# Optimization experiments

Hardware: AMD Instinct MI355X
Metric: run time of the kernel (lower is better)

## Reference

```python
import jax, jax.numpy as jnp
import numpy as np

B = 131072
NUM_MODS = 6
NUM_PREDS = 30
CLS_TH = 2.0
CLS_IGNORE = 0.2
MGN = 0.2
CLS_COEF = 1.0
REG_COEF = 1.0


def setup_inputs() -> dict:
    key = jax.random.key(0)
    k1, k2, k3 = jax.random.split(key, 3)
    reg = jax.random.normal(k1, (B, NUM_MODS, NUM_PREDS, 2), jnp.float32)
    cls = jax.random.normal(k2, (B, NUM_MODS), jnp.float32)
    gt_preds = jax.random.normal(k3, (B, NUM_PREDS, 2), jnp.float32)
    has_preds = jnp.ones((B, NUM_PREDS), dtype=bool)
    return {"reg": reg, "cls": cls, "gt_preds": gt_preds, "has_preds": has_preds}


def _loss(reg, cls, gt, has):
    # ---------------- PredLoss (LaneGCN cls + reg loss) ----------------
    hasf = has.astype(jnp.float32)
    last = hasf + 0.1 * jnp.arange(NUM_PREDS, dtype=jnp.float32) / float(NUM_PREDS)
    last_idcs = jnp.argmax(last, axis=1)                      # [B]
    max_last = jnp.max(last, axis=1)
    valid = max_last > 1.0                                    # [B] rows kept by `mask`

    # distance of each mode's last-valid point to gt last-valid point
    reg_last = jnp.take_along_axis(reg, last_idcs[:, None, None, None], axis=2)[:, :, 0, :]  # [B,6,2]
    gt_last = jnp.take_along_axis(gt, last_idcs[:, None, None], axis=1)[:, 0, :]             # [B,2]
    dist = jnp.sqrt(((reg_last - gt_last[:, None, :]) ** 2).sum(-1))                          # [B,6]

    min_idcs = jnp.argmin(dist, axis=1)                       # [B]
    min_dist = jnp.min(dist, axis=1)

    cls_min = jnp.take_along_axis(cls, min_idcs[:, None], axis=1)  # [B,1]
    mgn = cls_min - cls                                            # [B,6]
    m01 = (min_dist < CLS_TH)[:, None] & ((dist - min_dist[:, None]) > CLS_IGNORE) & valid[:, None]
    cls_mask = m01 & (mgn < MGN)
    num_cls = cls_mask.sum()
    cls_loss = CLS_COEF * (MGN * num_cls.astype(jnp.float32) - jnp.where(cls_mask, mgn, 0.0).sum())

    # SmoothL1 (beta=1, reduction='sum') over best mode, masked by has & valid
    reg_best = jnp.take_along_axis(reg, min_idcs[:, None, None, None], axis=1)[:, 0]  # [B,30,2]
    diff = reg_best - gt
    ad = jnp.abs(diff)
    sl1 = jnp.where(ad < 1.0, 0.5 * diff * diff, ad - 0.5)
    w = (has & valid[:, None]).astype(jnp.float32)[..., None]  # [B,30,1]
    reg_loss = REG_COEF * (sl1 * w).sum()
    num_reg = (has & valid[:, None]).sum()

    loss = cls_loss / (num_cls.astype(jnp.float32) + 1e-10) + reg_loss / (num_reg.astype(jnp.float32) + 1e-10)

    # ---------------- heading (vectorized over scenes) ----------------
    gx, gy = gt[..., 0], gt[..., 1]                           # [B,30]
    fwd = jnp.arctan2(gy[:, 2:] - gy[:, 1:-1], gx[:, 2:] - gx[:, 1:-1])   # [B,28]
    bwd = jnp.arctan2(gy[:, 1:-1] - gy[:, :-2], gx[:, 1:-1] - gx[:, :-2]) # [B,28]
    head_tmp = jnp.rad2deg(fwd) + jnp.rad2deg(bwd)                         # [B,28]
    mid = jnp.where((fwd == 0.0) | (bwd == 0.0), head_tmp, head_tmp / 2.0)
    head0 = jnp.rad2deg(jnp.arctan2(gy[:, 1] - gy[:, 0], gx[:, 1] - gx[:, 0]))
    headL = jnp.rad2deg(jnp.arctan2(gy[:, -1] - gy[:, -2], gx[:, -1] - gx[:, -2]))
    head = jnp.concatenate([head0[:, None], mid, headL[:, None]], axis=1)  # [B,30]
    moving = jnp.sqrt(((gt[:, 0, :] - gt[:, -1, :]) ** 2).sum(-1)) > 2.0
    head = jnp.where(moving[:, None], head, 0.0)

    # ---------------- rotated dist_error (per-timestep 2x2 rotation) ----------------
    de0 = jnp.abs(gt[:, None, :, :] - reg)                    # [B,6,30,2] L1Loss(reduction='none')
    theta = jnp.deg2rad(-head)                                # [B,30]
    c = jnp.cos(theta)[:, None, :]                            # [B,1,30]
    s = jnp.sin(theta)[:, None, :]
    dx, dy = de0[..., 0], de0[..., 1]                         # [B,6,30]
    rx = c * dx - s * dy
    ry = s * dx + c * dy
    de = jnp.abs(jnp.stack([rx, ry], axis=-1))                # [B,6,30,2]

    top1 = jnp.argmax(cls, axis=1)                            # [B]
    de_top = jnp.take_along_axis(de, top1[:, None, None, None], axis=1)[:, 0]  # [B,30,2]

    ade6_x = de[..., 0].sum(); ade6_y = de[..., 1].sum()
    fde6_x = de[:, :, -1, 0].sum(); fde6_y = de[:, :, -1, 1].sum()
    ade1_x = de_top[..., 0].sum(); ade1_y = de_top[..., 1].sum()
    fde1_x = de_top[:, -1, 0].sum(); fde1_y = de_top[:, -1, 1].sum()

    Bn = de.shape[0]
    counts = jnp.array([
        NUM_MODS * Bn * NUM_PREDS,  # ade6_num
        NUM_MODS * Bn,              # fde6_num
        Bn * NUM_PREDS,             # ade1_num
        Bn,                         # fde1_num
    ], dtype=jnp.float32)

    return jnp.stack([
        loss, cls_loss, num_cls.astype(jnp.float32), reg_loss, num_reg.astype(jnp.float32),
        ade6_x, ade6_y, fde6_x, fde6_y, counts[0], counts[1],
        ade1_x, ade1_y, fde1_x, fde1_y, counts[2], counts[3],
    ])


def reference(reg, cls, gt_preds, has_preds):
    return _loss(reg, cls, gt_preds, has_preds)
```

## Files before the change

kernel.cpp:

```cpp
#include <hip/hip_runtime.h>
#include <hip/hip_bf16.h>
#include <math.h>

#define B_ROWS 131072
#define NMODS 6
#define NPREDS 30


__device__ __forceinline__ float wave_reduce(float v) {
    v += __shfl_xor(v, 32);
    v += __shfl_xor(v, 16);
    v += __shfl_xor(v, 8);
    v += __shfl_xor(v, 4);
    v += __shfl_xor(v, 2);
    v += __shfl_xor(v, 1);
    return v;
}

__global__ __launch_bounds__(256) void loss_main(
    const float* __restrict__ reg,
    const float* __restrict__ cls,
    const float* __restrict__ gt,
    const int* __restrict__ has,
    float* __restrict__ acc)
{
    const int lane = threadIdx.x & 63;
    const int wid  = threadIdx.x >> 6;
    const int gw   = blockIdx.x * 4 + wid;
    const int nw   = gridDim.x * 4;

    float ade6x = 0.f, ade6y = 0.f, fde6x = 0.f, fde6y = 0.f;
    float ade1x = 0.f, ade1y = 0.f, fde1x = 0.f, fde1y = 0.f;
    float regloss = 0.f, summgn = 0.f, numcls = 0.f, numreg = 0.f;

    for (int b = gw; b < B_ROWS; b += nw) {
        bool hp = false;
        if (lane < NPREDS) hp = (has[b * NPREDS + lane] != 0);
        unsigned long long mask = __ballot(hp);
        int last_idx = mask ? (63 - __builtin_clzll(mask)) : (NPREDS - 1);
        bool valid = (mask & ~1ull) != 0ull;

        float gx = 0.f, gy = 0.f;
        if (lane < NPREDS) {
            const float2 g = ((const float2*)gt)[b * NPREDS + lane];
            gx = g.x; gy = g.y;
        }

        float gxn = __shfl(gx, (lane + 1) & 63);
        float gyn = __shfl(gy, (lane + 1) & 63);
        float seg = 0.f;
        if (lane < NPREDS - 1) seg = atan2f(gyn - gy, gxn - gx);
        float segp  = __shfl(seg, (lane + 63) & 63);
        float seg28 = __shfl(seg, NPREDS - 2);

        float gx0  = __shfl(gx, 0),          gy0  = __shfl(gy, 0);
        float gx29 = __shfl(gx, NPREDS - 1), gy29 = __shfl(gy, NPREDS - 1);
        float mdx = gx0 - gx29, mdy = gy0 - gy29;
        bool moving = (mdx * mdx + mdy * mdy) > 4.0f;

        float head;
        if (lane == 0)                head = seg;
        else if (lane >= NPREDS - 1)  head = seg28;
        else                          head = (seg == 0.f || segp == 0.f)
                                             ? (seg + segp) : 0.5f * (seg + segp);
        if (!moving) head = 0.f;
        float ct = cosf(-head);
        float st = sinf(-head);

        float glx = __shfl(gx, last_idx);
        float gly = __shfl(gy, last_idx);
        float d = 0.f;
        if (lane < NMODS) {
            const float2 rl = ((const float2*)reg)[(size_t)(b * NMODS + lane) * NPREDS + last_idx];
            float dxm = rl.x - glx, dym = rl.y - gly;
            d = sqrtf(dxm * dxm + dym * dym);
        }
        float d0 = __shfl(d, 0), d1 = __shfl(d, 1), d2 = __shfl(d, 2);
        float d3 = __shfl(d, 3), d4 = __shfl(d, 4), d5 = __shfl(d, 5);
        float mind = d0; int mini = 0;
        if (d1 < mind) { mind = d1; mini = 1; }
        if (d2 < mind) { mind = d2; mini = 2; }
        if (d3 < mind) { mind = d3; mini = 3; }
        if (d4 < mind) { mind = d4; mini = 4; }
        if (d5 < mind) { mind = d5; mini = 5; }

        float cm = (lane < NMODS) ? cls[b * NMODS + lane] : 0.f;
        float clsmin = __shfl(cm, mini);
        if (lane < NMODS) {
            float mgn = clsmin - cm;
            if (valid && (mind < 2.0f) && ((d - mind) > 0.2f) && (mgn < 0.2f)) {
                numcls += 1.0f;
                summgn += mgn;
            }
        }

        float c0 = __shfl(cm, 0), c1 = __shfl(cm, 1), c2 = __shfl(cm, 2);
        float c3 = __shfl(cm, 3), c4 = __shfl(cm, 4), c5 = __shfl(cm, 5);
        float bestc = c0; int top1 = 0;
        if (c1 > bestc) { bestc = c1; top1 = 1; }
        if (c2 > bestc) { bestc = c2; top1 = 2; }
        if (c3 > bestc) { bestc = c3; top1 = 3; }
        if (c4 > bestc) { bestc = c4; top1 = 4; }
        if (c5 > bestc) { bestc = c5; top1 = 5; }

        if (lane == 0 && valid) numreg += (float)__builtin_popcountll(mask);

        const float2* regrow = ((const float2*)reg) + (size_t)b * (NMODS * NPREDS);
        #pragma unroll
        for (int it = 0; it < 3; ++it) {
            int p = lane + it * 64;
            int m = p / NPREDS;
            int t = p - m * NPREDS;
            int ts = (p < NMODS * NPREDS) ? t : 0;
            float gxt = __shfl(gx, ts);
            float gyt = __shfl(gy, ts);
            float ctt = __shfl(ct, ts);
            float stt = __shfl(st, ts);
            if (p < NMODS * NPREDS) {
                float2 rv = regrow[p];
                float dx = fabsf(gxt - rv.x);
                float dy = fabsf(gyt - rv.y);
                float ax = fabsf(ctt * dx - stt * dy);
                float ay = fabsf(stt * dx + ctt * dy);
                ade6x += ax; ade6y += ay;
                if (t == NPREDS - 1) { fde6x += ax; fde6y += ay; }
                if (m == top1) {
                    ade1x += ax; ade1y += ay;
                    if (t == NPREDS - 1) { fde1x += ax; fde1y += ay; }
                }
                if (m == mini && valid && ((mask >> t) & 1ull)) {
                    float e0 = rv.x - gxt;
                    float e1 = rv.y - gyt;
                    float a0 = fabsf(e0), a1 = fabsf(e1);
                    regloss += (a0 < 1.f) ? (0.5f * e0 * e0) : (a0 - 0.5f);
                    regloss += (a1 < 1.f) ? (0.5f * e1 * e1) : (a1 - 0.5f);
                }
            }
        }
    }

    float vals[12] = { ade6x, ade6y, fde6x, fde6y, ade1x, ade1y, fde1x, fde1y,
                       regloss, summgn, numcls, numreg };
    #pragma unroll
    for (int i = 0; i < 12; ++i) vals[i] = wave_reduce(vals[i]);

    __shared__ float blk[4][12];
    if (lane == 0) {
        #pragma unroll
        for (int i = 0; i < 12; ++i) blk[wid][i] = vals[i];
    }
    __syncthreads();
    if (threadIdx.x < 12) {
        float s = blk[0][threadIdx.x] + blk[1][threadIdx.x]
                + blk[2][threadIdx.x] + blk[3][threadIdx.x];
        atomicAdd(&acc[threadIdx.x], s);
    }
}

__global__ void finalize(const float* __restrict__ acc, float* __restrict__ out) {
    if (threadIdx.x == 0) {
        float nc = acc[10], nr = acc[11];
        float cls_loss = 0.2f * nc - acc[9];
        float reg_loss = acc[8];
        float loss = cls_loss / (nc + 1e-10f) + reg_loss / (nr + 1e-10f);
        out[0]  = loss;
        out[1]  = cls_loss;
        out[2]  = nc;
        out[3]  = reg_loss;
        out[4]  = nr;
        out[5]  = acc[0];
        out[6]  = acc[1];
        out[7]  = acc[2];
        out[8]  = acc[3];
        out[9]  = 23592960.0f;
        out[10] = 786432.0f;
        out[11] = acc[4];
        out[12] = acc[5];
        out[13] = acc[6];
        out[14] = acc[7];
        out[15] = 3932160.0f;
        out[16] = 131072.0f;
    }
}

extern "C" void kernel_launch(void* const* d_in, const int* in_sizes, int n_in,
                              void* d_out, int out_size, void* d_ws, size_t ws_size,
                              hipStream_t stream) {
    const float* reg = (const float*)d_in[0];
    const float* cls = (const float*)d_in[1];
    const float* gt  = (const float*)d_in[2];
    const int*   has = (const int*)d_in[3];
    float* out = (float*)d_out;
    float* acc = (float*)d_ws;

    hipMemsetAsync(acc, 0, 12 * sizeof(float), stream);
    loss_main<<<2048, 256, 0, stream>>>(reg, cls, gt, has, acc);
    finalize<<<1, 64, 0, stream>>>(acc, out);
}
```

Baseline: 375.3 us.

## Remap loss kernel from one wave per row to one thread per row

The kernel now gives each thread one whole row instead of one 64-lane wave per row. It builds the has-mask with int2 loads instead of a ballot, and computes headings and cos/sin serially in registers, packed as half2, instead of through many cross-lane shuffles. The reg row is read with float4 loads and the per-mode conditional branches become multiply-by-flag accumulation. This removes the shuffle overhead and idle lanes of the wave-per-row scheme. In exchange, global loads are strided across lanes, per-thread register use is high, only 2048 waves run, and gt and the rotations are held in half precision with fast sin/cos, which costs accuracy.

```diff
diff --git a/kernel.cpp b/kernel.cpp
--- a/kernel.cpp
+++ b/kernel.cpp
@@ -1,5 +1,5 @@
 #include <hip/hip_runtime.h>
-#include <hip/hip_bf16.h>
+#include <hip/hip_fp16.h>
 #include <math.h>
 
 #define B_ROWS 131072
@@ -17,120 +17,134 @@
     return v;
 }
 
-__global__ __launch_bounds__(256) void loss_main(
+__global__ __launch_bounds__(256) void loss_lane(
     const float* __restrict__ reg,
     const float* __restrict__ cls,
     const float* __restrict__ gt,
     const int* __restrict__ has,
     float* __restrict__ acc)
 {
-    const int lane = threadIdx.x & 63;
-    const int wid  = threadIdx.x >> 6;
-    const int gw   = blockIdx.x * 4 + wid;
-    const int nw   = gridDim.x * 4;
+    const int r = blockIdx.x * 256 + threadIdx.x;
+
+    const int2* h2 = (const int2*)(has + (size_t)r * NPREDS);
+    unsigned mask = 0u;
+    #pragma unroll
+    for (int i = 0; i < 15; ++i) {
+        int2 h = h2[i];
+        mask |= (h.x != 0 ? 1u : 0u) << (2 * i);
+        mask |= (h.y != 0 ? 1u : 0u) << (2 * i + 1);
+    }
+    const int  last_idx = mask ? (31 - __builtin_clz(mask)) : (NPREDS - 1);
+    const bool valid    = (mask & ~1u) != 0u;
+
+    const float2* grow = (const float2*)(gt + (size_t)r * NPREDS * 2);
+    float2 g0  = grow[0];
+    float2 g29 = grow[NPREDS - 1];
+    float mdx = g0.x - g29.x, mdy = g0.y - g29.y;
+    const bool moving = (mdx * mdx + mdy * mdy) > 4.0f;
+
+    __half2 gxy[NPREDS];
+    __half2 ctst[NPREDS];
+
+    float cx = g0.x, cy = g0.y;
+    float seg_prev = 0.f;
+    #pragma unroll
+    for (int t = 0; t < NPREDS; ++t) {
+        float nx = cx, ny = cy;
+        if (t < NPREDS - 1) { float2 gn = grow[t + 1]; nx = gn.x; ny = gn.y; }
+        gxy[t] = __floats2half2_rn(cx, cy);
+
+        float head;
+        if (t == 0) {
+            float seg = atan2f(ny - cy, nx - cx);
+            head = seg;
+            seg_prev = seg;
+        } else if (t < NPREDS - 1) {
+            float seg = atan2f(ny - cy, nx - cx);
+            head = (seg == 0.f || seg_prev == 0.f) ? (seg + seg_prev)
+                                                   : 0.5f * (seg + seg_prev);
+            seg_prev = seg;
+        } else {
+            head = seg_prev;
+        }
+        if (!moving) head = 0.f;
+        float th = -head;
+        ctst[t] = __floats2half2_rn(__cosf(th), __sinf(th));
+        cx = nx; cy = ny;
+    }
+
+    float2 gl = grow[last_idx];
+    const float2* rbase = (const float2*)(reg + (size_t)r * NMODS * NPREDS * 2);
+    float dists[NMODS];
+    #pragma unroll
+    for (int m = 0; m < NMODS; ++m) {
+        float2 rl = rbase[m * NPREDS + last_idx];
+        float ddx = rl.x - gl.x, ddy = rl.y - gl.y;
+        dists[m] = sqrtf(ddx * ddx + ddy * ddy);
+    }
+    float mind = dists[0]; int mini = 0;
+    #pragma unroll
+    for (int m = 1; m < NMODS; ++m)
+        if (dists[m] < mind) { mind = dists[m]; mini = m; }
+
+    const float2* c2p = (const float2*)(cls + (size_t)r * NMODS);
+    float cv[NMODS];
+    #pragma unroll
+    for (int i = 0; i < 3; ++i) { float2 c2 = c2p[i]; cv[2 * i] = c2.x; cv[2 * i + 1] = c2.y; }
+
+    float clsmin = cv[0];
+    #pragma unroll
+    for (int m = 1; m < NMODS; ++m) clsmin = (m == mini) ? cv[m] : clsmin;
+
+    float numcls_l = 0.f, summgn_l = 0.f;
+    if (valid && (mind < 2.0f)) {
+        #pragma unroll
+        for (int m = 0; m < NMODS; ++m) {
+            float mgn = clsmin - cv[m];
+            if (((dists[m] - mind) > 0.2f) && (mgn < 0.2f)) {
+                numcls_l += 1.0f;
+                summgn_l += mgn;
+            }
+        }
+    }
+
+    float bc = cv[0]; int top1 = 0;
+    #pragma unroll
+    for (int m = 1; m < NMODS; ++m)
+        if (cv[m] > bc) { bc = cv[m]; top1 = m; }
+
+    float numreg_l = valid ? (float)__builtin_popcount(mask) : 0.f;
 
     float ade6x = 0.f, ade6y = 0.f, fde6x = 0.f, fde6y = 0.f;
     float ade1x = 0.f, ade1y = 0.f, fde1x = 0.f, fde1y = 0.f;
-    float regloss = 0.f, summgn = 0.f, numcls = 0.f, numreg = 0.f;
-
-    for (int b = gw; b < B_ROWS; b += nw) {
-        bool hp = false;
-        if (lane < NPREDS) hp = (has[b * NPREDS + lane] != 0);
-        unsigned long long mask = __ballot(hp);
-        int last_idx = mask ? (63 - __builtin_clzll(mask)) : (NPREDS - 1);
-        bool valid = (mask & ~1ull) != 0ull;
-
-        float gx = 0.f, gy = 0.f;
-        if (lane < NPREDS) {
-            const float2 g = ((const float2*)gt)[b * NPREDS + lane];
-            gx = g.x; gy = g.y;
-        }
-
-        float gxn = __shfl(gx, (lane + 1) & 63);
-        float gyn = __shfl(gy, (lane + 1) & 63);
-        float seg = 0.f;
-        if (lane < NPREDS - 1) seg = atan2f(gyn - gy, gxn - gx);
-        float segp  = __shfl(seg, (lane + 63) & 63);
-        float seg28 = __shfl(seg, NPREDS - 2);
-
-        float gx0  = __shfl(gx, 0),          gy0  = __shfl(gy, 0);
-        float gx29 = __shfl(gx, NPREDS - 1), gy29 = __shfl(gy, NPREDS - 1);
-        float mdx = gx0 - gx29, mdy = gy0 - gy29;
-        bool moving = (mdx * mdx + mdy * mdy) > 4.0f;
-
-        float head;
-        if (lane == 0)                head = seg;
-        else if (lane >= NPREDS - 1)  head = seg28;
-        else                          head = (seg == 0.f || segp == 0.f)
-                                             ? (seg + segp) : 0.5f * (seg + segp);
-        if (!moving) head = 0.f;
-        float ct = cosf(-head);
-        float st = sinf(-head);
-
-        float glx = __shfl(gx, last_idx);
-        float gly = __shfl(gy, last_idx);
-        float d = 0.f;
-        if (lane < NMODS) {
-            const float2 rl = ((const float2*)reg)[(size_t)(b * NMODS + lane) * NPREDS + last_idx];
-            float dxm = rl.x - glx, dym = rl.y - gly;
-            d = sqrtf(dxm * dxm + dym * dym);
-        }
-        float d0 = __shfl(d, 0), d1 = __shfl(d, 1), d2 = __shfl(d, 2);
-        float d3 = __shfl(d, 3), d4 = __shfl(d, 4), d5 = __shfl(d, 5);
-        float mind = d0; int mini = 0;
-        if (d1 < mind) { mind = d1; mini = 1; }
-        if (d2 < mind) { mind = d2; mini = 2; }
-        if (d3 < mind) { mind = d3; mini = 3; }
-        if (d4 < mind) { mind = d4; mini = 4; }
-        if (d5 < mind) { mind = d5; mini = 5; }
-
-        float cm = (lane < NMODS) ? cls[b * NMODS + lane] : 0.f;
-        float clsmin = __shfl(cm, mini);
-        if (lane < NMODS) {
-            float mgn = clsmin - cm;
-            if (valid && (mind < 2.0f) && ((d - mind) > 0.2f) && (mgn < 0.2f)) {
-                numcls += 1.0f;
-                summgn += mgn;
-            }
-        }
-
-        float c0 = __shfl(cm, 0), c1 = __shfl(cm, 1), c2 = __shfl(cm, 2);
-        float c3 = __shfl(cm, 3), c4 = __shfl(cm, 4), c5 = __shfl(cm, 5);
-        float bestc = c0; int top1 = 0;
-        if (c1 > bestc) { bestc = c1; top1 = 1; }
-        if (c2 > bestc) { bestc = c2; top1 = 2; }
-        if (c3 > bestc) { bestc = c3; top1 = 3; }
-        if (c4 > bestc) { bestc = c4; top1 = 4; }
-        if (c5 > bestc) { bestc = c5; top1 = 5; }
-
-        if (lane == 0 && valid) numreg += (float)__builtin_popcountll(mask);
-
-        const float2* regrow = ((const float2*)reg) + (size_t)b * (NMODS * NPREDS);
+    float regloss = 0.f;
+
+    const float4* r4 = (const float4*)rbase;
+    #pragma unroll
+    for (int m = 0; m < NMODS; ++m) {
+        const float topf = (m == top1) ? 1.f : 0.f;
+        const bool  best = (m == mini) && valid;
         #pragma unroll
-        for (int it = 0; it < 3; ++it) {
-            int p = lane + it * 64;
-            int m = p / NPREDS;
-            int t = p - m * NPREDS;
-            int ts = (p < NMODS * NPREDS) ? t : 0;
-            float gxt = __shfl(gx, ts);
-            float gyt = __shfl(gy, ts);
-            float ctt = __shfl(ct, ts);
-            float stt = __shfl(st, ts);
-            if (p < NMODS * NPREDS) {
-                float2 rv = regrow[p];
-                float dx = fabsf(gxt - rv.x);
-                float dy = fabsf(gyt - rv.y);
-                float ax = fabsf(ctt * dx - stt * dy);
-                float ay = fabsf(stt * dx + ctt * dy);
+        for (int q = 0; q < 15; ++q) {
+            float4 v = r4[m * 15 + q];
+            #pragma unroll
+            for (int half = 0; half < 2; ++half) {
+                const int t = 2 * q + half;
+                const float rx = half ? v.z : v.x;
+                const float ry = half ? v.w : v.y;
+                float gxt = __low2float(gxy[t]),  gyt = __high2float(gxy[t]);
+                float ct  = __low2float(ctst[t]), st  = __high2float(ctst[t]);
+                float dx = fabsf(gxt - rx), dy = fabsf(gyt - ry);
+                float ax = fabsf(ct * dx - st * dy);
+                float ay = fabsf(st * dx + ct * dy);
                 ade6x += ax; ade6y += ay;
-                if (t == NPREDS - 1) { fde6x += ax; fde6y += ay; }
-                if (m == top1) {
-                    ade1x += ax; ade1y += ay;
-                    if (t == NPREDS - 1) { fde1x += ax; fde1y += ay; }
+                ade1x += topf * ax; ade1y += topf * ay;
+                if (t == NPREDS - 1) {
+                    fde6x += ax; fde6y += ay;
+                    fde1x += topf * ax; fde1y += topf * ay;
                 }
-                if (m == mini && valid && ((mask >> t) & 1ull)) {
-                    float e0 = rv.x - gxt;
-                    float e1 = rv.y - gyt;
+                if (best && ((mask >> t) & 1u)) {
+                    float e0 = rx - gxt, e1 = ry - gyt;
                     float a0 = fabsf(e0), a1 = fabsf(e1);
                     regloss += (a0 < 1.f) ? (0.5f * e0 * e0) : (a0 - 0.5f);
                     regloss += (a1 < 1.f) ? (0.5f * e1 * e1) : (a1 - 0.5f);
@@ -140,11 +154,13 @@
     }
 
     float vals[12] = { ade6x, ade6y, fde6x, fde6y, ade1x, ade1y, fde1x, fde1y,
-                       regloss, summgn, numcls, numreg };
+                       regloss, summgn_l, numcls_l, numreg_l };
     #pragma unroll
     for (int i = 0; i < 12; ++i) vals[i] = wave_reduce(vals[i]);
 
     __shared__ float blk[4][12];
+    const int lane = threadIdx.x & 63;
+    const int wid  = threadIdx.x >> 6;
     if (lane == 0) {
         #pragma unroll
         for (int i = 0; i < 12; ++i) blk[wid][i] = vals[i];
@@ -194,6 +210,6 @@
     float* acc = (float*)d_ws;
 
     hipMemsetAsync(acc, 0, 12 * sizeof(float), stream);
-    loss_main<<<2048, 256, 0, stream>>>(reg, cls, gt, has, acc);
+    loss_lane<<<B_ROWS / 256, 256, 0, stream>>>(reg, cls, gt, has, acc);
     finalize<<<1, 64, 0, stream>>>(acc, out);
 }
```

Result: slower. 412.7 us (+10.0%).
